# Optimization experiments

Hardware: AMD Instinct MI355X
Metric: run time of the kernel (lower is better)

The kernel has to match this reference:

```python
import jax, jax.numpy as jnp
import numpy as np

N, W, D, IC, OC, R = 256, 1, 64, 32, 32, 8


def setup_inputs() -> dict:
    key = jax.random.key(0)
    k1, k2 = jax.random.split(key)
    x = jax.random.normal(k1, (N, W, D, IC, R), dtype=jnp.float32)
    weights = jax.random.normal(k2, (D, IC, OC, R), dtype=jnp.float32)
    return {"x": x, "weights": weights}


def reference(x, weights):
    # x: [n, w, d, ic, r] -> [n, w, d, ic, 1, r]
    # weights: [d, ic, oc, r] -> broadcast as [1, 1, d, ic, oc, r]
    # out: logsumexp over ic -> [n, w, d, oc, r]
    logits = x[:, :, :, :, None, :] + weights[None, None]
    return jax.nn.logsumexp(logits, axis=3)
```

## Files before the change

kernel.cpp:

```cpp
#include <hip/hip_runtime.h>


typedef __attribute__((ext_vector_type(8))) short bf16x8;
typedef __attribute__((ext_vector_type(4))) float f32x4;

constexpr int kD = 64, kIC = 32, kOC = 32, kR = 8;
constexpr int kNT = 32;

__device__ __forceinline__ unsigned short f2bf(float f) {
    unsigned u = __builtin_bit_cast(unsigned, f);
    u += 0x7FFFu + ((u >> 16) & 1u);
    return (unsigned short)(u >> 16);
}

__global__ __launch_bounds__(256) void lse_kernel(
    const float* __restrict__ x, const float* __restrict__ w,
    float* __restrict__ out)
{
    __shared__ __align__(16) unsigned short xs[2 * 8 * 64 * 8];
    __shared__ __align__(16) unsigned short wsm[2 * 8 * 64 * 8];

    const int t  = threadIdx.x;
    const int d  = blockIdx.x;
    const int n0 = blockIdx.y * kNT;

    const int c  = t & 7;
    const int ch = c & 1;
    const int cq = c >> 1;
    const int nl = t >> 3;

    const float* xrow = x + (size_t)(n0 + nl) * (kD * kIC * kR) + (size_t)d * (kIC * kR);
    const float* wd   = w + (size_t)d * (kIC * kOC * kR);
    float4 xv[8], wv[8];
    #pragma unroll
    for (int a = 0; a < 4; ++a) {
        const int ic0 = 8 * a + 2 * cq;
        xv[2*a]   = *reinterpret_cast<const float4*>(xrow + ic0 * 8 + 4 * ch);
        xv[2*a+1] = *reinterpret_cast<const float4*>(xrow + ic0 * 8 + 8 + 4 * ch);
        wv[2*a]   = *reinterpret_cast<const float4*>(wd + (size_t)ic0 * 256 + nl * 8 + 4 * ch);
        wv[2*a+1] = *reinterpret_cast<const float4*>(wd + (size_t)(ic0 + 1) * 256 + nl * 8 + 4 * ch);
    }

    {
        const int row = nl & 15, tt = nl >> 4, s0 = 2 * cq;
        #pragma unroll
        for (int a = 0; a < 4; ++a)
            #pragma unroll
            for (int j = 0; j < 4; ++j) {
                const int r = 4 * ch + j;
                const unsigned pk =
                    (unsigned)f2bf(__expf(reinterpret_cast<const float*>(&xv[2*a])[j])) |
                    ((unsigned)f2bf(__expf(reinterpret_cast<const float*>(&xv[2*a+1])[j])) << 16);
                *reinterpret_cast<unsigned*>(&xs[((tt * 8 + r) * 64 + a * 16 + row) * 8 + s0]) = pk;
            }
    }
    {
        const int col = nl & 15, u = nl >> 4, s0 = 2 * cq;
        #pragma unroll
        for (int a = 0; a < 4; ++a)
            #pragma unroll
            for (int j = 0; j < 4; ++j) {
                const int r = 4 * ch + j;
                const unsigned pk =
                    (unsigned)f2bf(__expf(reinterpret_cast<const float*>(&wv[2*a])[j])) |
                    ((unsigned)f2bf(__expf(reinterpret_cast<const float*>(&wv[2*a+1])[j])) << 16);
                *reinterpret_cast<unsigned*>(&wsm[((u * 8 + r) * 64 + a * 16 + col) * 8 + s0]) = pk;
            }
    }

    __syncthreads();

    const int wave = t >> 6;
    const int wt = wave & 1;
    const int wu = wave >> 1;
    const int l  = t & 63;

    f32x4 acc[8];
    #pragma unroll
    for (int r = 0; r < 8; ++r) {
        bf16x8 av = *reinterpret_cast<const bf16x8*>(&xs[(wt * 8 + r) * 512 + l * 8]);
        bf16x8 bv = *reinterpret_cast<const bf16x8*>(&wsm[(wu * 8 + r) * 512 + l * 8]);
        f32x4 z = {0.f, 0.f, 0.f, 0.f};
        acc[r] = __builtin_amdgcn_mfma_f32_16x16x32_bf16(av, bv, z, 0, 0, 0);
    }

    const int colL = l & 15, qL = l >> 4;
    float* opb = out + (size_t)d * (kOC * kR) + (size_t)(wu * 16 + colL) * 8;
    #pragma unroll
    for (int i = 0; i < 4; ++i) {
        const int n = n0 + wt * 16 + qL * 4 + i;
        float* op = opb + (size_t)n * (kD * kOC * kR);
        float4 v0, v1;
        v0.x = __logf(acc[0][i]); v0.y = __logf(acc[1][i]);
        v0.z = __logf(acc[2][i]); v0.w = __logf(acc[3][i]);
        v1.x = __logf(acc[4][i]); v1.y = __logf(acc[5][i]);
        v1.z = __logf(acc[6][i]); v1.w = __logf(acc[7][i]);
        *reinterpret_cast<float4*>(op)     = v0;
        *reinterpret_cast<float4*>(op + 4) = v1;
    }
}

extern "C" void kernel_launch(void* const* d_in, const int* in_sizes, int n_in,
                              void* d_out, int out_size, void* d_ws, size_t ws_size,
                              hipStream_t stream) {
    const float* x = (const float*)d_in[0];
    const float* w = (const float*)d_in[1];
    float* out = (float*)d_out;
    dim3 grid(kD, 256 / kNT);
    lse_kernel<<<grid, 256, 0, stream>>>(x, w, out);
}
```

Before: 13.54 us.

## Split x staging into two halves and overlap second half with first compute

The block's 32 rows of x are staged into shared memory as two 16-row halves. The first half is converted and synced, its MFMAs are computed, and the second half's exp/bf16 conversion and store are interleaved with the first half's log and global store before a second barrier. Waves are re-partitioned by output column half and r-quarter instead of n-half. The goal is to overlap staging, compute and output stores, at the cost of an extra __syncthreads and changed access and store patterns (16-byte stores instead of 32-byte per row).

```diff
diff --git a/kernel.cpp b/kernel.cpp
--- a/kernel.cpp
+++ b/kernel.cpp
@@ -5,7 +5,6 @@
 typedef __attribute__((ext_vector_type(4))) float f32x4;
 
 constexpr int kD = 64, kIC = 32, kOC = 32, kR = 8;
-constexpr int kNT = 32;
 
 __device__ __forceinline__ unsigned short f2bf(float f) {
     unsigned u = __builtin_bit_cast(unsigned, f);
@@ -17,50 +16,43 @@
     const float* __restrict__ x, const float* __restrict__ w,
     float* __restrict__ out)
 {
+    __shared__ __align__(16) unsigned short wsm[2 * 8 * 64 * 8];
     __shared__ __align__(16) unsigned short xs[2 * 8 * 64 * 8];
-    __shared__ __align__(16) unsigned short wsm[2 * 8 * 64 * 8];
 
     const int t  = threadIdx.x;
     const int d  = blockIdx.x;
-    const int n0 = blockIdx.y * kNT;
+    const int n0 = blockIdx.y * 32;
 
-    const int c  = t & 7;
-    const int ch = c & 1;
-    const int cq = c >> 1;
-    const int nl = t >> 3;
-
-    const float* xrow = x + (size_t)(n0 + nl) * (kD * kIC * kR) + (size_t)d * (kIC * kR);
-    const float* wd   = w + (size_t)d * (kIC * kOC * kR);
-    float4 xv[8], wv[8];
+    const int cw = t & 7, chw = cw & 1, cqw = cw >> 1, ol = t >> 3;
+    const float* wd = w + (size_t)d * (kIC * kOC * kR);
+    float4 wv[8];
     #pragma unroll
     for (int a = 0; a < 4; ++a) {
-        const int ic0 = 8 * a + 2 * cq;
-        xv[2*a]   = *reinterpret_cast<const float4*>(xrow + ic0 * 8 + 4 * ch);
-        xv[2*a+1] = *reinterpret_cast<const float4*>(xrow + ic0 * 8 + 8 + 4 * ch);
-        wv[2*a]   = *reinterpret_cast<const float4*>(wd + (size_t)ic0 * 256 + nl * 8 + 4 * ch);
-        wv[2*a+1] = *reinterpret_cast<const float4*>(wd + (size_t)(ic0 + 1) * 256 + nl * 8 + 4 * ch);
+        const int ic0 = 8 * a + 2 * cqw;
+        wv[2*a]   = *reinterpret_cast<const float4*>(wd + (size_t)ic0 * 256 + ol * 8 + 4 * chw);
+        wv[2*a+1] = *reinterpret_cast<const float4*>(wd + (size_t)(ic0 + 1) * 256 + ol * 8 + 4 * chw);
+    }
+
+    const int cx = t & 15, e = cx & 1, icp = cx >> 1, nlx = t >> 4;
+    const float* xr0 = x + (size_t)(n0 + nlx) * (kD * kIC * kR) + (size_t)d * (kIC * kR);
+    const float* xr1 = xr0 + (size_t)16 * (kD * kIC * kR);
+    float4 x0v[4], x1v[4];
+    #pragma unroll
+    for (int a = 0; a < 2; ++a) {
+        const int ic0 = 16 * a + 2 * icp;
+        x0v[2*a]   = *reinterpret_cast<const float4*>(xr0 + ic0 * 8 + 4 * e);
+        x0v[2*a+1] = *reinterpret_cast<const float4*>(xr0 + ic0 * 8 + 8 + 4 * e);
+        x1v[2*a]   = *reinterpret_cast<const float4*>(xr1 + ic0 * 8 + 4 * e);
+        x1v[2*a+1] = *reinterpret_cast<const float4*>(xr1 + ic0 * 8 + 8 + 4 * e);
     }
 
     {
-        const int row = nl & 15, tt = nl >> 4, s0 = 2 * cq;
+        const int col = ol & 15, u = ol >> 4, s0 = 2 * cqw;
         #pragma unroll
         for (int a = 0; a < 4; ++a)
             #pragma unroll
             for (int j = 0; j < 4; ++j) {
-                const int r = 4 * ch + j;
-                const unsigned pk =
-                    (unsigned)f2bf(__expf(reinterpret_cast<const float*>(&xv[2*a])[j])) |
-                    ((unsigned)f2bf(__expf(reinterpret_cast<const float*>(&xv[2*a+1])[j])) << 16);
-                *reinterpret_cast<unsigned*>(&xs[((tt * 8 + r) * 64 + a * 16 + row) * 8 + s0]) = pk;
-            }
-    }
-    {
-        const int col = nl & 15, u = nl >> 4, s0 = 2 * cq;
-        #pragma unroll
-        for (int a = 0; a < 4; ++a)
-            #pragma unroll
-            for (int j = 0; j < 4; ++j) {
-                const int r = 4 * ch + j;
+                const int r = 4 * chw + j;
                 const unsigned pk =
                     (unsigned)f2bf(__expf(reinterpret_cast<const float*>(&wv[2*a])[j])) |
                     ((unsigned)f2bf(__expf(reinterpret_cast<const float*>(&wv[2*a+1])[j])) << 16);
@@ -68,36 +60,63 @@
             }
     }
 
+    const int icg = 2 * 0 + 0; (void)icg;
+    auto stage_x = [&](int c, const float4* xcv) {
+        const int ig_lo = icp >> 2;
+        const int s0x = 2 * (icp & 3);
+        #pragma unroll
+        for (int a = 0; a < 2; ++a) {
+            const int g = 2 * a + ig_lo;
+            const int lane = g * 16 + nlx;
+            #pragma unroll
+            for (int j = 0; j < 4; ++j) {
+                const int r = 4 * e + j;
+                const unsigned pk =
+                    (unsigned)f2bf(__expf(reinterpret_cast<const float*>(&xcv[2*a])[j])) |
+                    ((unsigned)f2bf(__expf(reinterpret_cast<const float*>(&xcv[2*a+1])[j])) << 16);
+                *reinterpret_cast<unsigned*>(&xs[((c * 8 + r) * 64 + lane) * 8 + s0x]) = pk;
+            }
+        }
+    };
+
+    stage_x(0, x0v);
     __syncthreads();
 
     const int wave = t >> 6;
-    const int wt = wave & 1;
-    const int wu = wave >> 1;
+    const int wu = wave & 1;
+    const int wr = wave >> 1;
     const int l  = t & 63;
+    const int colL = l & 15, qL = l >> 4;
 
-    f32x4 acc[8];
-    #pragma unroll
-    for (int r = 0; r < 8; ++r) {
-        bf16x8 av = *reinterpret_cast<const bf16x8*>(&xs[(wt * 8 + r) * 512 + l * 8]);
-        bf16x8 bv = *reinterpret_cast<const bf16x8*>(&wsm[(wu * 8 + r) * 512 + l * 8]);
-        f32x4 z = {0.f, 0.f, 0.f, 0.f};
-        acc[r] = __builtin_amdgcn_mfma_f32_16x16x32_bf16(av, bv, z, 0, 0, 0);
-    }
+    f32x4 acc0[4], acc1[4];
+    auto compute = [&](int c, f32x4* acc) {
+        #pragma unroll
+        for (int j = 0; j < 4; ++j) {
+            const int r = wr * 4 + j;
+            bf16x8 av = *reinterpret_cast<const bf16x8*>(&xs[((c * 8 + r) * 64 + l) * 8]);
+            bf16x8 bv = *reinterpret_cast<const bf16x8*>(&wsm[((wu * 8 + r) * 64 + l) * 8]);
+            f32x4 z = {0.f, 0.f, 0.f, 0.f};
+            acc[j] = __builtin_amdgcn_mfma_f32_16x16x32_bf16(av, bv, z, 0, 0, 0);
+        }
+    };
+    auto logstore = [&](int c, const f32x4* acc) {
+        #pragma unroll
+        for (int i = 0; i < 4; ++i) {
+            const int n = n0 + c * 16 + qL * 4 + i;
+            float4 v;
+            v.x = __logf(acc[0][i]); v.y = __logf(acc[1][i]);
+            v.z = __logf(acc[2][i]); v.w = __logf(acc[3][i]);
+            *reinterpret_cast<float4*>(out + (size_t)n * (kD * kOC * kR)
+                + (size_t)d * (kOC * kR) + (size_t)(wu * 16 + colL) * 8 + wr * 4) = v;
+        }
+    };
 
-    const int colL = l & 15, qL = l >> 4;
-    float* opb = out + (size_t)d * (kOC * kR) + (size_t)(wu * 16 + colL) * 8;
-    #pragma unroll
-    for (int i = 0; i < 4; ++i) {
-        const int n = n0 + wt * 16 + qL * 4 + i;
-        float* op = opb + (size_t)n * (kD * kOC * kR);
-        float4 v0, v1;
-        v0.x = __logf(acc[0][i]); v0.y = __logf(acc[1][i]);
-        v0.z = __logf(acc[2][i]); v0.w = __logf(acc[3][i]);
-        v1.x = __logf(acc[4][i]); v1.y = __logf(acc[5][i]);
-        v1.z = __logf(acc[6][i]); v1.w = __logf(acc[7][i]);
-        *reinterpret_cast<float4*>(op)     = v0;
-        *reinterpret_cast<float4*>(op + 4) = v1;
-    }
+    compute(0, acc0);
+    stage_x(1, x1v);
+    logstore(0, acc0);
+    __syncthreads();
+    compute(1, acc1);
+    logstore(1, acc1);
 }
 
 extern "C" void kernel_launch(void* const* d_in, const int* in_sizes, int n_in,
@@ -106,6 +125,6 @@
     const float* x = (const float*)d_in[0];
     const float* w = (const float*)d_in[1];
     float* out = (float*)d_out;
-    dim3 grid(kD, 256 / kNT);
+    dim3 grid(kD, 8);
     lse_kernel<<<grid, 256, 0, stream>>>(x, w, out);
 }
```

New measurement: 12.96 us. -4.2%, faster.

## Split R dimension across a third grid axis to double block count

Applied to the files above, without the earlier changes.

Adds a grid z-dimension that splits the 8-element R axis into two halves, so each block handles 4 r values instead of 8. This doubles the number of blocks (1024 instead of 512), halves per-thread loads, exp work and shared memory per block, and halves the MFMA count per wave. The aim is better occupancy and latency hiding across CUs. The cost is that each block fetches narrower float4 segments and writes half-width output rows, which may reduce coalescing.

```diff
diff --git a/kernel.cpp b/kernel.cpp
--- a/kernel.cpp
+++ b/kernel.cpp
@@ -5,98 +5,85 @@
 typedef __attribute__((ext_vector_type(4))) float f32x4;
 
 constexpr int kD = 64, kIC = 32, kOC = 32, kR = 8;
-constexpr int kNT = 32;
 
 __device__ __forceinline__ unsigned short f2bf(float f) {
     unsigned u = __builtin_bit_cast(unsigned, f);
     u += 0x7FFFu + ((u >> 16) & 1u);
     return (unsigned short)(u >> 16);
 }
+__device__ __forceinline__ unsigned pk2(float a, float b) {
+    return (unsigned)f2bf(a) | ((unsigned)f2bf(b) << 16);
+}
 
 __global__ __launch_bounds__(256) void lse_kernel(
     const float* __restrict__ x, const float* __restrict__ w,
     float* __restrict__ out)
 {
-    __shared__ __align__(16) unsigned short xs[2 * 8 * 64 * 8];
-    __shared__ __align__(16) unsigned short wsm[2 * 8 * 64 * 8];
+    __shared__ __align__(16) unsigned short wsm[2 * 4 * 64 * 8];
+    __shared__ __align__(16) unsigned short xs [2 * 4 * 64 * 8];
 
     const int t  = threadIdx.x;
     const int d  = blockIdx.x;
-    const int n0 = blockIdx.y * kNT;
+    const int n0 = blockIdx.y * 32;
+    const int rh = blockIdx.z;
 
     const int c  = t & 7;
-    const int ch = c & 1;
-    const int cq = c >> 1;
-    const int nl = t >> 3;
+    const int hi = t >> 3;
 
-    const float* xrow = x + (size_t)(n0 + nl) * (kD * kIC * kR) + (size_t)d * (kIC * kR);
-    const float* wd   = w + (size_t)d * (kIC * kOC * kR);
-    float4 xv[8], wv[8];
+    const float* wd = w + (size_t)d * (kIC * kOC * kR);
+    const float* xr = x + (size_t)(n0 + hi) * (kD * kIC * kR) + (size_t)d * (kIC * kR);
+    float4 wv[2][2], xv[2][2];
     #pragma unroll
-    for (int a = 0; a < 4; ++a) {
-        const int ic0 = 8 * a + 2 * cq;
-        xv[2*a]   = *reinterpret_cast<const float4*>(xrow + ic0 * 8 + 4 * ch);
-        xv[2*a+1] = *reinterpret_cast<const float4*>(xrow + ic0 * 8 + 8 + 4 * ch);
-        wv[2*a]   = *reinterpret_cast<const float4*>(wd + (size_t)ic0 * 256 + nl * 8 + 4 * ch);
-        wv[2*a+1] = *reinterpret_cast<const float4*>(wd + (size_t)(ic0 + 1) * 256 + nl * 8 + 4 * ch);
-    }
+    for (int a = 0; a < 2; ++a)
+        #pragma unroll
+        for (int p = 0; p < 2; ++p) {
+            const int ic = 2 * c + 16 * a + p;
+            wv[a][p] = *reinterpret_cast<const float4*>(wd + (size_t)ic * 256 + hi * 8 + rh * 4);
+            xv[a][p] = *reinterpret_cast<const float4*>(xr + ic * 8 + rh * 4);
+        }
 
-    {
-        const int row = nl & 15, tt = nl >> 4, s0 = 2 * cq;
+    const int g0 = c >> 2, s = 2 * (c & 3);
+    const int col = hi & 15, u = hi >> 4;
+    #pragma unroll
+    for (int a = 0; a < 2; ++a) {
+        const int g = g0 + 2 * a;
         #pragma unroll
-        for (int a = 0; a < 4; ++a)
-            #pragma unroll
-            for (int j = 0; j < 4; ++j) {
-                const int r = 4 * ch + j;
-                const unsigned pk =
-                    (unsigned)f2bf(__expf(reinterpret_cast<const float*>(&xv[2*a])[j])) |
-                    ((unsigned)f2bf(__expf(reinterpret_cast<const float*>(&xv[2*a+1])[j])) << 16);
-                *reinterpret_cast<unsigned*>(&xs[((tt * 8 + r) * 64 + a * 16 + row) * 8 + s0]) = pk;
-            }
-    }
-    {
-        const int col = nl & 15, u = nl >> 4, s0 = 2 * cq;
-        #pragma unroll
-        for (int a = 0; a < 4; ++a)
-            #pragma unroll
-            for (int j = 0; j < 4; ++j) {
-                const int r = 4 * ch + j;
-                const unsigned pk =
-                    (unsigned)f2bf(__expf(reinterpret_cast<const float*>(&wv[2*a])[j])) |
-                    ((unsigned)f2bf(__expf(reinterpret_cast<const float*>(&wv[2*a+1])[j])) << 16);
-                *reinterpret_cast<unsigned*>(&wsm[((u * 8 + r) * 64 + a * 16 + col) * 8 + s0]) = pk;
-            }
+        for (int j = 0; j < 4; ++j) {
+            const float* w0 = reinterpret_cast<const float*>(&wv[a][0]);
+            const float* w1 = reinterpret_cast<const float*>(&wv[a][1]);
+            const float* x0 = reinterpret_cast<const float*>(&xv[a][0]);
+            const float* x1 = reinterpret_cast<const float*>(&xv[a][1]);
+            *reinterpret_cast<unsigned*>(&wsm[((u * 4 + j) * 64 + g * 16 + col) * 8 + s]) =
+                pk2(__expf(w0[j]), __expf(w1[j]));
+            *reinterpret_cast<unsigned*>(&xs[((u * 4 + j) * 64 + g * 16 + col) * 8 + s]) =
+                pk2(__expf(x0[j]), __expf(x1[j]));
+        }
     }
 
     __syncthreads();
 
     const int wave = t >> 6;
-    const int wt = wave & 1;
-    const int wu = wave >> 1;
+    const int wt = wave & 1, wu = wave >> 1;
     const int l  = t & 63;
 
-    f32x4 acc[8];
+    f32x4 acc[4];
     #pragma unroll
-    for (int r = 0; r < 8; ++r) {
-        bf16x8 av = *reinterpret_cast<const bf16x8*>(&xs[(wt * 8 + r) * 512 + l * 8]);
-        bf16x8 bv = *reinterpret_cast<const bf16x8*>(&wsm[(wu * 8 + r) * 512 + l * 8]);
+    for (int j = 0; j < 4; ++j) {
+        bf16x8 av = *reinterpret_cast<const bf16x8*>(&xs [((wt * 4 + j) * 64 + l) * 8]);
+        bf16x8 bv = *reinterpret_cast<const bf16x8*>(&wsm[((wu * 4 + j) * 64 + l) * 8]);
         f32x4 z = {0.f, 0.f, 0.f, 0.f};
-        acc[r] = __builtin_amdgcn_mfma_f32_16x16x32_bf16(av, bv, z, 0, 0, 0);
+        acc[j] = __builtin_amdgcn_mfma_f32_16x16x32_bf16(av, bv, z, 0, 0, 0);
     }
 
     const int colL = l & 15, qL = l >> 4;
-    float* opb = out + (size_t)d * (kOC * kR) + (size_t)(wu * 16 + colL) * 8;
     #pragma unroll
     for (int i = 0; i < 4; ++i) {
         const int n = n0 + wt * 16 + qL * 4 + i;
-        float* op = opb + (size_t)n * (kD * kOC * kR);
-        float4 v0, v1;
-        v0.x = __logf(acc[0][i]); v0.y = __logf(acc[1][i]);
-        v0.z = __logf(acc[2][i]); v0.w = __logf(acc[3][i]);
-        v1.x = __logf(acc[4][i]); v1.y = __logf(acc[5][i]);
-        v1.z = __logf(acc[6][i]); v1.w = __logf(acc[7][i]);
-        *reinterpret_cast<float4*>(op)     = v0;
-        *reinterpret_cast<float4*>(op + 4) = v1;
+        float4 v;
+        v.x = __logf(acc[0][i]); v.y = __logf(acc[1][i]);
+        v.z = __logf(acc[2][i]); v.w = __logf(acc[3][i]);
+        *reinterpret_cast<float4*>(out + (size_t)n * (kD * kOC * kR)
+            + (size_t)d * (kOC * kR) + (size_t)(wu * 16 + colL) * 8 + rh * 4) = v;
     }
 }
 
@@ -106,6 +93,6 @@
     const float* x = (const float*)d_in[0];
     const float* w = (const float*)d_in[1];
     float* out = (float*)d_out;
-    dim3 grid(kD, 256 / kNT);
+    dim3 grid(kD, 8, 2);
     lse_kernel<<<grid, 256, 0, stream>>>(x, w, out);
 }
```

Measured after the change: 14.85 us. +9.7%, slower.
